# Kernel tuning notes

Hardware: AMD Instinct MI355X
Metric: run time of the kernel (lower is better)

Reference implementation:

```python
import jax, jax.numpy as jnp
import numpy as np

NUM_HEADS = 16


def setup_inputs() -> dict:
    key = jax.random.key(0)
    ks = jax.random.split(key, 6)
    B, N, M, C = 2, 2048, 2048, 1024
    return {
        "reference_data": jax.random.normal(ks[0], (B, N, C), dtype=jnp.float32),
        "target_data": jax.random.normal(ks[1], (B, M, C), dtype=jnp.float32),
        "Wq": jax.random.normal(ks[2], (C, C), dtype=jnp.float32) * (C ** -0.5),
        "Wkv": jax.random.normal(ks[3], (C, 2 * C), dtype=jnp.float32) * (C ** -0.5),
        "Wproj": jax.random.normal(ks[4], (C, C), dtype=jnp.float32) * (C ** -0.5),
        "bproj": jnp.zeros((C,), dtype=jnp.float32),
    }


def reference(reference_data, target_data, Wq, Wkv, Wproj, bproj):
    B, N, C = reference_data.shape
    M = target_data.shape[1]
    H = NUM_HEADS
    hd = C // H
    scale = hd ** -0.5
    # k, v from reference: [B, N, 2, H, hd] -> two [B, H, N, hd]
    kv = (reference_data @ Wkv).reshape(B, N, 2, H, hd)
    k = jnp.transpose(kv[:, :, 0], (0, 2, 1, 3))  # [B,H,N,hd]
    v = jnp.transpose(kv[:, :, 1], (0, 2, 1, 3))  # [B,H,N,hd]
    # q from target: [B, H, M, hd]
    q = jnp.transpose((target_data @ Wq).reshape(B, M, H, hd), (0, 2, 1, 3))
    attn = jnp.einsum("bhid,bhjd->bhij", q, k) * scale  # [B,H,M,N]
    attn = jax.nn.softmax(attn, axis=-1)
    x = jnp.einsum("bhij,bhjd->bhid", attn, v)  # [B,H,M,hd]
    x = jnp.transpose(x, (0, 2, 1, 3)).reshape(B, M, C)
    return x @ Wproj + bproj
```

## Files before the change

kernel.cpp:

```cpp
#include <hip/hip_runtime.h>
#include <hip/hip_bf16.h>
#include <stdint.h>

#define SEQ   2048
#define CH    1024
#define NH    16
#define HD    64
#define NUMEL (2 * NH * SEQ * HD)

typedef short bf8 __attribute__((ext_vector_type(8)));
typedef short bf4 __attribute__((ext_vector_type(4)));
typedef float f4  __attribute__((ext_vector_type(4)));
typedef unsigned short u16;

#define GAS(p) ((const __attribute__((address_space(1))) void*)(p))
#define LAS(p) ((__attribute__((address_space(3))) void*)(p))

__device__ __forceinline__ u16 f2bf(float f) {
  uint32_t u = __float_as_uint(f);
  u += 0x7fffu + ((u >> 16) & 1u);
  return (u16)(u >> 16);
}

__device__ __forceinline__ float bf2f(u16 v) {
  return __uint_as_float(((uint32_t)v) << 16);
}

__device__ __forceinline__ uint32_t pk2bf(float a, float b) {
  float2 f; f.x = a; f.y = b;
  __hip_bfloat162 h = __float22bfloat162_rn(f);
  union { __hip_bfloat162 h; uint32_t u; } cv; cv.h = h;
  return cv.u;
}

__device__ __forceinline__ f4 MFMA32(bf8 a, bf8 b, f4 c) {
  return __builtin_amdgcn_mfma_f32_16x16x32_bf16(a, b, c, 0, 0, 0);
}

__device__ __forceinline__ f4 MFMA16(bf4 a, bf4 b, f4 c) {
#if __has_builtin(__builtin_amdgcn_mfma_f32_16x16x16_bf16)
  return __builtin_amdgcn_mfma_f32_16x16x16_bf16(a, b, c, 0, 0, 0);
#elif __has_builtin(__builtin_amdgcn_mfma_f32_16x16x16bf16_1k)
  return __builtin_amdgcn_mfma_f32_16x16x16bf16_1k(a, b, c, 0, 0, 0);
#else
  f4 d = c;
  asm volatile("v_mfma_f32_16x16x16_bf16 %0, %1, %2, %0"
               : "+v"(d) : "v"(a), "v"(b));
  return d;
#endif
}

__global__ void prep(const float* __restrict__ ref, u16* __restrict__ refb,
                     const float* __restrict__ tgt, u16* __restrict__ tgtb,
                     const float* __restrict__ Wq, u16* __restrict__ Wqt,
                     const float* __restrict__ Wkv, u16* __restrict__ Wkvt,
                     const float* __restrict__ Wp, u16* __restrict__ Wpt) {
  __shared__ float tile[32][33];
  int blk = blockIdx.x;
  int t = threadIdx.x;
  if (blk < 8192) {
    const float* in; u16* out;
    if (blk < 4096) { in = ref; out = refb; } else { in = tgt; out = tgtb; blk -= 4096; }
    int i = (blk * 256 + t) * 4;
    float4 f = *reinterpret_cast<const float4*>(in + i);
    ushort4 o;
    o.x = f2bf(f.x); o.y = f2bf(f.y); o.z = f2bf(f.z); o.w = f2bf(f.w);
    *reinterpret_cast<ushort4*>(out + i) = o;
    return;
  }
  blk -= 8192;
  int x = blk & 127, by = blk >> 7;
  const float* in; u16* out; int N;
  if (x < 32)       { in = Wq;  out = Wqt;  N = CH;     }
  else if (x < 96)  { in = Wkv; out = Wkvt; N = 2 * CH; x -= 32; }
  else              { in = Wp;  out = Wpt;  N = CH;     x -= 96; }
  const int K = CH;
  int bn = x * 32, bk = by * 32;
  int tx = t & 31, ty = t >> 5;
  #pragma unroll
  for (int i = ty; i < 32; i += 8)
    tile[i][tx] = in[(size_t)(bk + i) * N + bn + tx];
  __syncthreads();
  #pragma unroll
  for (int i = ty; i < 32; i += 8)
    out[(size_t)(bn + i) * K + bk + tx] = f2bf(tile[tx][i]);
}

__global__ __launch_bounds__(256, 3)
void gemm_qkv(const u16* __restrict__ tgtb, const u16* __restrict__ refb,
              const u16* __restrict__ Wqt, const u16* __restrict__ Wkvt,
              u16* __restrict__ qb, u16* __restrict__ karr, u16* __restrict__ varr)
{
  __shared__ __align__(16) u16 As[2][4096];
  __shared__ __align__(16) u16 Bs[2][4096];
  const int tid = threadIdx.x;
  const int lane = tid & 63, wave = tid >> 6;
  const int l16 = lane & 15, q = lane >> 4;
  const int blk = blockIdx.x;
  const int n_idx = blk >> 5, m_idx = blk & 31;
  const bool isQ = n_idx >= 16;
  const u16* A  = isQ ? tgtb : refb;
  const u16* Bt = isQ ? Wqt : Wkvt;
  const int n0 = (isQ ? (n_idx - 16) : n_idx) * 128;
  const int m0 = m_idx * 128;
  const int wm = (wave >> 1) * 64, wn = (wave & 1) * 64;
  const int Kdim = CH;
  const int c = tid, c2 = tid + 256;
  const int ar = c >> 2, ac = (c & 3) << 3, ar2 = c2 >> 2, ac2 = (c2 & 3) << 3;

  f4 acc[4][4] = {};

  #define STAGE_G(buf, k0)                                                      \
    { __builtin_amdgcn_global_load_lds(                                         \
          GAS(&A[(size_t)(m0 + ar) * Kdim + (k0) + ac]),                        \
          LAS(&As[buf][c << 3]), 16, 0, 0);                                     \
      __builtin_amdgcn_global_load_lds(                                         \
          GAS(&A[(size_t)(m0 + ar2) * Kdim + (k0) + ac2]),                      \
          LAS(&As[buf][c2 << 3]), 16, 0, 0);                                    \
      __builtin_amdgcn_global_load_lds(                                         \
          GAS(&Bt[(size_t)(n0 + ar) * Kdim + (k0) + ac]),                       \
          LAS(&Bs[buf][c << 3]), 16, 0, 0);                                     \
      __builtin_amdgcn_global_load_lds(                                         \
          GAS(&Bt[(size_t)(n0 + ar2) * Kdim + (k0) + ac2]),                     \
          LAS(&Bs[buf][c2 << 3]), 16, 0, 0); }

  STAGE_G(0, 0);
  for (int kk = 0; kk < 32; ++kk) {
    __syncthreads();
    if (kk < 31) STAGE_G((kk + 1) & 1, (kk + 1) * 32);
    const u16* as = As[kk & 1];
    const u16* bs = Bs[kk & 1];
    bf8 a[4], b[4];
    #pragma unroll
    for (int i = 0; i < 4; ++i)
      a[i] = *reinterpret_cast<const bf8*>(&as[(wm + i * 16 + l16) * 32 + q * 8]);
    #pragma unroll
    for (int j = 0; j < 4; ++j)
      b[j] = *reinterpret_cast<const bf8*>(&bs[(wn + j * 16 + l16) * 32 + q * 8]);
    #pragma unroll
    for (int i = 0; i < 4; ++i)
      #pragma unroll
      for (int j = 0; j < 4; ++j)
        acc[i][j] = MFMA32(a[i], b[j], acc[i][j]);
  }
  #undef STAGE_G

  #pragma unroll
  for (int i = 0; i < 4; ++i) {
    const int mbase = m0 + wm + i * 16 + q * 4;
    const int b = mbase >> 11, ns0 = mbase & (SEQ - 1);
    #pragma unroll
    for (int j = 0; j < 4; ++j) {
      const int n = n0 + wn + j * 16 + l16;
      if (isQ) {
        int h = n >> 6, d = n & 63;
        #pragma unroll
        for (int r = 0; r < 4; ++r)
          qb[(size_t)((b * NH + h) * SEQ + ns0 + r) * HD + d] =
              f2bf(acc[i][j][r] * 0.1803368801f);
      } else if (n < CH) {
        int h = n >> 6, d = n & 63;
        size_t base = (size_t)(b * NH + h) * SEQ * HD;
        int off = (((ns0 >> 4) * 2 + (d >> 5)) * 4 + ((d >> 3) & 3)) * 128
                  + (d & 7);
        #pragma unroll
        for (int r = 0; r < 4; ++r)
          karr[base + off + ((ns0 + r) & 15) * 8] = f2bf(acc[i][j][r]);
      } else {
        int c2v = n - CH, h = c2v >> 6, d = c2v & 63;
        size_t base = (size_t)(b * NH + h) * SEQ * HD;
        int off = (((ns0 >> 4) * 2 + (d >> 5)) * 4 + ((ns0 >> 2) & 3)) * 128
                  + (d & 15) * 8 + ((d >> 4) & 1) * 4;
        ushort4 st;
        st.x = f2bf(acc[i][j][0]); st.y = f2bf(acc[i][j][1]);
        st.z = f2bf(acc[i][j][2]); st.w = f2bf(acc[i][j][3]);
        *reinterpret_cast<ushort4*>(&varr[base + off]) = st;
      }
    }
  }
}

__global__ __launch_bounds__(256, 2)
void gemm_proj(const u16* __restrict__ A, const u16* __restrict__ Bt,
               float* __restrict__ fo, const float* __restrict__ bias)
{
  __shared__ __align__(16) u16 As[2][2048];
  __shared__ __align__(16) u16 Bs[2][4096];
  const int tid = threadIdx.x;
  const int lane = tid & 63, wave = tid >> 6;
  const int l16 = lane & 15, q = lane >> 4;
  const int blk = blockIdx.x;
  const int m0 = (blk & 63) * 64, n0 = (blk >> 6) * 128;
  const int wm = (wave >> 1) * 32, wn = (wave & 1) * 64;
  const int Kdim = CH;
  const int c = tid, c2 = tid + 256;
  const int ar = c >> 2, ac = (c & 3) << 3, ar2 = c2 >> 2, ac2 = (c2 & 3) << 3;
  const int aar = c >> 2, aac = (c & 3) << 3;

  f4 acc[2][4] = {};

  #define STAGE_P(buf, k0)                                                      \
    { __builtin_amdgcn_global_load_lds(                                         \
          GAS(&A[(size_t)(m0 + aar) * Kdim + (k0) + aac]),                      \
          LAS(&As[buf][c << 3]), 16, 0, 0);                                     \
      __builtin_amdgcn_global_load_lds(                                         \
          GAS(&Bt[(size_t)(n0 + ar) * Kdim + (k0) + ac]),                       \
          LAS(&Bs[buf][c << 3]), 16, 0, 0);                                     \
      __builtin_amdgcn_global_load_lds(                                         \
          GAS(&Bt[(size_t)(n0 + ar2) * Kdim + (k0) + ac2]),                     \
          LAS(&Bs[buf][c2 << 3]), 16, 0, 0); }

  STAGE_P(0, 0);
  for (int kk = 0; kk < 32; ++kk) {
    __syncthreads();
    if (kk < 31) STAGE_P((kk + 1) & 1, (kk + 1) * 32);
    const u16* as = As[kk & 1];
    const u16* bs = Bs[kk & 1];
    bf8 a[2], b[4];
    #pragma unroll
    for (int i = 0; i < 2; ++i)
      a[i] = *reinterpret_cast<const bf8*>(&as[(wm + i * 16 + l16) * 32 + q * 8]);
    #pragma unroll
    for (int j = 0; j < 4; ++j)
      b[j] = *reinterpret_cast<const bf8*>(&bs[(wn + j * 16 + l16) * 32 + q * 8]);
    #pragma unroll
    for (int i = 0; i < 2; ++i)
      #pragma unroll
      for (int j = 0; j < 4; ++j)
        acc[i][j] = MFMA32(a[i], b[j], acc[i][j]);
  }
  #undef STAGE_P

  #pragma unroll
  for (int i = 0; i < 2; ++i) {
    const int mbase = m0 + wm + i * 16 + q * 4;
    #pragma unroll
    for (int j = 0; j < 4; ++j) {
      const int n = n0 + wn + j * 16 + l16;
      #pragma unroll
      for (int r = 0; r < 4; ++r)
        fo[(size_t)(mbase + r) * CH + n] = acc[i][j][r] + bias[n];
    }
  }
}

__global__ __launch_bounds__(512, 8)
void attn(const u16* __restrict__ Q, const u16* __restrict__ Karr,
          const u16* __restrict__ Varr, u16* __restrict__ num,
          float* __restrict__ den)
{
  __shared__ __align__(16) u16 Ks[8192];
  __shared__ __align__(16) u16 Vs[8192];
  const int tid = threadIdx.x;
  const int lane = tid & 63;
  const int l16 = lane & 15, q = lane >> 4;
  const int bh = blockIdx.y;
  const int m0 = blockIdx.x * 128;
  const int sp = blockIdx.z;
  const int wm = (tid >> 6) * 16;

  const u16* Qb = Q    + (size_t)bh * SEQ * HD;
  const u16* Kb = Karr + (size_t)bh * SEQ * HD;
  const u16* Vb = Varr + (size_t)bh * SEQ * HD;

  bf8 qf[2];
  #pragma unroll
  for (int ks = 0; ks < 2; ++ks)
    qf[ks] = *reinterpret_cast<const bf8*>(
        &Qb[(size_t)(m0 + wm + l16) * HD + ks * 32 + q * 8]);

  const short one_bf = 0x3F80;
  const bf4 ones = {one_bf, one_bf, one_bf, one_bf};

  f4 o[4] = {};
  f4 ds = {};

  const int t0 = sp * 8;
  for (int t = 0; t < 8; ++t) {
    const int tt = t0 + t;
    __syncthreads();
    {
      const u16* kg = Kb + (size_t)tt * 8192;
      const u16* vg = Vb + (size_t)tt * 8192;
      #pragma unroll
      for (int s = 0; s < 2; ++s) {
        int cc = tid + s * 512;
        __builtin_amdgcn_global_load_lds(GAS(kg + cc * 8), LAS(&Ks[cc * 8]), 16, 0, 0);
        __builtin_amdgcn_global_load_lds(GAS(vg + cc * 8), LAS(&Vs[cc * 8]), 16, 0, 0);
      }
    }
    __syncthreads();

    bf4 pa[8];
    #pragma unroll
    for (int j = 0; j < 8; ++j) {
      bf8 kf0 = *reinterpret_cast<const bf8*>(&Ks[((j * 2 + 0) * 4 + q) * 128 + l16 * 8]);
      bf8 kf1 = *reinterpret_cast<const bf8*>(&Ks[((j * 2 + 1) * 4 + q) * 128 + l16 * 8]);
      f4 z = {};
      z = MFMA32(kf0, qf[0], z);
      z = MFMA32(kf1, qf[1], z);
      union { bf4 v; uint32_t u[2]; } w;
      w.u[0] = pk2bf(exp2f(z[0]), exp2f(z[1]));
      w.u[1] = pk2bf(exp2f(z[2]), exp2f(z[3]));
      pa[j] = w.v;
    }

    #pragma unroll
    for (int j = 0; j < 8; ++j) {
      ds = MFMA16(pa[j], ones, ds);
      #pragma unroll
      for (int dh = 0; dh < 2; ++dh) {
        bf8 vv = *reinterpret_cast<const bf8*>(&Vs[((j * 2 + dh) * 4 + q) * 128 + l16 * 8]);
        bf4 v0 = __builtin_shufflevector(vv, vv, 0, 1, 2, 3);
        bf4 v1 = __builtin_shufflevector(vv, vv, 4, 5, 6, 7);
        o[dh * 2 + 0] = MFMA16(pa[j], v0, o[dh * 2 + 0]);
        o[dh * 2 + 1] = MFMA16(pa[j], v1, o[dh * 2 + 1]);
      }
    }
  }

  u16* nh = num + (size_t)sp * NUMEL;
  float* dh_ = den + (size_t)sp * (2 * NH * SEQ);
  #pragma unroll
  for (int r = 0; r < 4; ++r) {
    int m = m0 + wm + q * 4 + r;
    if (l16 == 0) dh_[bh * SEQ + m] = ds[r];
    #pragma unroll
    for (int dt = 0; dt < 4; ++dt)
      nh[((size_t)bh * SEQ + m) * HD + dt * 16 + l16] = f2bf(o[dt][r]);
  }
}

__global__ void combine(const u16* __restrict__ num, const float* __restrict__ den,
                        u16* __restrict__ xb) {
  int idx = (blockIdx.x * 256 + threadIdx.x) * 4;
  int bh = idx >> 17;
  int rem = idx & (SEQ * HD - 1);
  int m = rem >> 6, d = rem & 63;
  ushort4 a = *reinterpret_cast<const ushort4*>(num + idx);
  ushort4 b4 = *reinterpret_cast<const ushort4*>(num + NUMEL + idx);
  float dsum = den[bh * SEQ + m] + den[2 * NH * SEQ + bh * SEQ + m];
  float inv = 1.0f / dsum;
  int b = bh >> 4, h = bh & (NH - 1);
  ushort4 o;
  o.x = f2bf((bf2f(a.x) + bf2f(b4.x)) * inv);
  o.y = f2bf((bf2f(a.y) + bf2f(b4.y)) * inv);
  o.z = f2bf((bf2f(a.z) + bf2f(b4.z)) * inv);
  o.w = f2bf((bf2f(a.w) + bf2f(b4.w)) * inv);
  *reinterpret_cast<ushort4*>(&xb[(size_t)(b * SEQ + m) * CH + h * HD + d]) = o;
}

extern "C" void kernel_launch(void* const* d_in, const int* in_sizes, int n_in,
                              void* d_out, int out_size, void* d_ws, size_t ws_size,
                              hipStream_t stream) {
  const float* ref   = (const float*)d_in[0];
  const float* tgt   = (const float*)d_in[1];
  const float* Wq    = (const float*)d_in[2];
  const float* Wkv   = (const float*)d_in[3];
  const float* Wproj = (const float*)d_in[4];
  const float* bproj = (const float*)d_in[5];
  float* out = (float*)d_out;

  char* ws = (char*)d_ws;
  u16* refb = (u16*)(ws);
  u16* tgtb = (u16*)(ws + (8  << 20));
  u16* Wqt  = (u16*)(ws + (16 << 20));
  u16* Wkvt = (u16*)(ws + (18 << 20));
  u16* Wpt  = (u16*)(ws + (22 << 20));
  u16* qb   = (u16*)(ws + (24 << 20));
  u16* karr = (u16*)(ws + (32 << 20));
  u16* varr = (u16*)(ws + (40 << 20));
  u16* xb   = (u16*)(ws + (48 << 20));
  u16* nbuf  = refb;
  float* dbuf = (float*)Wqt;

  prep<<<12288, 256, 0, stream>>>(ref, refb, tgt, tgtb, Wq, Wqt, Wkv, Wkvt, Wproj, Wpt);

  gemm_qkv<<<768, 256, 0, stream>>>(tgtb, refb, Wqt, Wkvt, qb, karr, varr);

  attn<<<dim3(16, 32, 2), 512, 0, stream>>>(qb, karr, varr, nbuf, dbuf);

  combine<<<4096, 256, 0, stream>>>(nbuf, dbuf, xb);

  gemm_proj<<<512, 256, 0, stream>>>(xb, Wpt, out, bproj);
}
```

Before: 217.2 us.

## Rebalance QKV GEMM to 512 threads and double attention rows per wave

The QKV GEMM now runs 512 threads per block, so each wave computes a 32x64 sub-tile and each thread issues a single staging load per operand. The attention kernel now has each wave handle two 16-row query groups over 256 query rows per block. This halves the number of blocks and reuses each K/V tile loaded into LDS for twice as many queries. The cost is more registers per thread in attention (occupancy hint lowered from 8 to 4) and fewer blocks to spread across the GPU.

```diff
diff --git a/kernel.cpp b/kernel.cpp
--- a/kernel.cpp
+++ b/kernel.cpp
@@ -86,7 +86,7 @@
     out[(size_t)(bn + i) * K + bk + tx] = f2bf(tile[tx][i]);
 }
 
-__global__ __launch_bounds__(256, 3)
+__global__ __launch_bounds__(512, 6)
 void gemm_qkv(const u16* __restrict__ tgtb, const u16* __restrict__ refb,
               const u16* __restrict__ Wqt, const u16* __restrict__ Wkvt,
               u16* __restrict__ qb, u16* __restrict__ karr, u16* __restrict__ varr)
@@ -103,26 +103,19 @@
   const u16* Bt = isQ ? Wqt : Wkvt;
   const int n0 = (isQ ? (n_idx - 16) : n_idx) * 128;
   const int m0 = m_idx * 128;
-  const int wm = (wave >> 1) * 64, wn = (wave & 1) * 64;
+  const int wm = (wave >> 1) * 32, wn = (wave & 1) * 64;
   const int Kdim = CH;
-  const int c = tid, c2 = tid + 256;
-  const int ar = c >> 2, ac = (c & 3) << 3, ar2 = c2 >> 2, ac2 = (c2 & 3) << 3;
-
-  f4 acc[4][4] = {};
+  const int ar = tid >> 2, ac = (tid & 3) << 3;
+
+  f4 acc[2][4] = {};
 
   #define STAGE_G(buf, k0)                                                      \
     { __builtin_amdgcn_global_load_lds(                                         \
           GAS(&A[(size_t)(m0 + ar) * Kdim + (k0) + ac]),                        \
-          LAS(&As[buf][c << 3]), 16, 0, 0);                                     \
-      __builtin_amdgcn_global_load_lds(                                         \
-          GAS(&A[(size_t)(m0 + ar2) * Kdim + (k0) + ac2]),                      \
-          LAS(&As[buf][c2 << 3]), 16, 0, 0);                                    \
+          LAS(&As[buf][tid << 3]), 16, 0, 0);                                   \
       __builtin_amdgcn_global_load_lds(                                         \
           GAS(&Bt[(size_t)(n0 + ar) * Kdim + (k0) + ac]),                       \
-          LAS(&Bs[buf][c << 3]), 16, 0, 0);                                     \
-      __builtin_amdgcn_global_load_lds(                                         \
-          GAS(&Bt[(size_t)(n0 + ar2) * Kdim + (k0) + ac2]),                     \
-          LAS(&Bs[buf][c2 << 3]), 16, 0, 0); }
+          LAS(&Bs[buf][tid << 3]), 16, 0, 0); }
 
   STAGE_G(0, 0);
   for (int kk = 0; kk < 32; ++kk) {
@@ -130,15 +123,15 @@
     if (kk < 31) STAGE_G((kk + 1) & 1, (kk + 1) * 32);
     const u16* as = As[kk & 1];
     const u16* bs = Bs[kk & 1];
-    bf8 a[4], b[4];
-    #pragma unroll
-    for (int i = 0; i < 4; ++i)
+    bf8 a[2], b[4];
+    #pragma unroll
+    for (int i = 0; i < 2; ++i)
       a[i] = *reinterpret_cast<const bf8*>(&as[(wm + i * 16 + l16) * 32 + q * 8]);
     #pragma unroll
     for (int j = 0; j < 4; ++j)
       b[j] = *reinterpret_cast<const bf8*>(&bs[(wn + j * 16 + l16) * 32 + q * 8]);
     #pragma unroll
-    for (int i = 0; i < 4; ++i)
+    for (int i = 0; i < 2; ++i)
       #pragma unroll
       for (int j = 0; j < 4; ++j)
         acc[i][j] = MFMA32(a[i], b[j], acc[i][j]);
@@ -146,7 +139,7 @@
   #undef STAGE_G
 
   #pragma unroll
-  for (int i = 0; i < 4; ++i) {
+  for (int i = 0; i < 2; ++i) {
     const int mbase = m0 + wm + i * 16 + q * 4;
     const int b = mbase >> 11, ns0 = mbase & (SEQ - 1);
     #pragma unroll
@@ -244,7 +237,7 @@
   }
 }
 
-__global__ __launch_bounds__(512, 8)
+__global__ __launch_bounds__(512, 4)
 void attn(const u16* __restrict__ Q, const u16* __restrict__ Karr,
           const u16* __restrict__ Varr, u16* __restrict__ num,
           float* __restrict__ den)
@@ -255,25 +248,27 @@
   const int lane = tid & 63;
   const int l16 = lane & 15, q = lane >> 4;
   const int bh = blockIdx.y;
-  const int m0 = blockIdx.x * 128;
+  const int m0 = blockIdx.x * 256;
   const int sp = blockIdx.z;
-  const int wm = (tid >> 6) * 16;
+  const int wm = (tid >> 6) * 32;
 
   const u16* Qb = Q    + (size_t)bh * SEQ * HD;
   const u16* Kb = Karr + (size_t)bh * SEQ * HD;
   const u16* Vb = Varr + (size_t)bh * SEQ * HD;
 
-  bf8 qf[2];
-  #pragma unroll
-  for (int ks = 0; ks < 2; ++ks)
-    qf[ks] = *reinterpret_cast<const bf8*>(
-        &Qb[(size_t)(m0 + wm + l16) * HD + ks * 32 + q * 8]);
+  bf8 qf[2][2];
+  #pragma unroll
+  for (int i = 0; i < 2; ++i)
+    #pragma unroll
+    for (int ks = 0; ks < 2; ++ks)
+      qf[i][ks] = *reinterpret_cast<const bf8*>(
+          &Qb[(size_t)(m0 + wm + i * 16 + l16) * HD + ks * 32 + q * 8]);
 
   const short one_bf = 0x3F80;
   const bf4 ones = {one_bf, one_bf, one_bf, one_bf};
 
-  f4 o[4] = {};
-  f4 ds = {};
+  f4 o[2][4] = {};
+  f4 ds[2] = {};
 
   const int t0 = sp * 8;
   for (int t = 0; t < 8; ++t) {
@@ -291,30 +286,38 @@
     }
     __syncthreads();
 
-    bf4 pa[8];
+    bf4 pa[2][8];
     #pragma unroll
     for (int j = 0; j < 8; ++j) {
       bf8 kf0 = *reinterpret_cast<const bf8*>(&Ks[((j * 2 + 0) * 4 + q) * 128 + l16 * 8]);
       bf8 kf1 = *reinterpret_cast<const bf8*>(&Ks[((j * 2 + 1) * 4 + q) * 128 + l16 * 8]);
-      f4 z = {};
-      z = MFMA32(kf0, qf[0], z);
-      z = MFMA32(kf1, qf[1], z);
-      union { bf4 v; uint32_t u[2]; } w;
-      w.u[0] = pk2bf(exp2f(z[0]), exp2f(z[1]));
-      w.u[1] = pk2bf(exp2f(z[2]), exp2f(z[3]));
-      pa[j] = w.v;
+      #pragma unroll
+      for (int i = 0; i < 2; ++i) {
+        f4 z = {};
+        z = MFMA32(kf0, qf[i][0], z);
+        z = MFMA32(kf1, qf[i][1], z);
+        union { bf4 v; uint32_t u[2]; } w;
+        w.u[0] = pk2bf(exp2f(z[0]), exp2f(z[1]));
+        w.u[1] = pk2bf(exp2f(z[2]), exp2f(z[3]));
+        pa[i][j] = w.v;
+      }
     }
 
     #pragma unroll
     for (int j = 0; j < 8; ++j) {
-      ds = MFMA16(pa[j], ones, ds);
+      #pragma unroll
+      for (int i = 0; i < 2; ++i)
+        ds[i] = MFMA16(pa[i][j], ones, ds[i]);
       #pragma unroll
       for (int dh = 0; dh < 2; ++dh) {
         bf8 vv = *reinterpret_cast<const bf8*>(&Vs[((j * 2 + dh) * 4 + q) * 128 + l16 * 8]);
         bf4 v0 = __builtin_shufflevector(vv, vv, 0, 1, 2, 3);
         bf4 v1 = __builtin_shufflevector(vv, vv, 4, 5, 6, 7);
-        o[dh * 2 + 0] = MFMA16(pa[j], v0, o[dh * 2 + 0]);
-        o[dh * 2 + 1] = MFMA16(pa[j], v1, o[dh * 2 + 1]);
+        #pragma unroll
+        for (int i = 0; i < 2; ++i) {
+          o[i][dh * 2 + 0] = MFMA16(pa[i][j], v0, o[i][dh * 2 + 0]);
+          o[i][dh * 2 + 1] = MFMA16(pa[i][j], v1, o[i][dh * 2 + 1]);
+        }
       }
     }
   }
@@ -322,13 +325,15 @@
   u16* nh = num + (size_t)sp * NUMEL;
   float* dh_ = den + (size_t)sp * (2 * NH * SEQ);
   #pragma unroll
-  for (int r = 0; r < 4; ++r) {
-    int m = m0 + wm + q * 4 + r;
-    if (l16 == 0) dh_[bh * SEQ + m] = ds[r];
-    #pragma unroll
-    for (int dt = 0; dt < 4; ++dt)
-      nh[((size_t)bh * SEQ + m) * HD + dt * 16 + l16] = f2bf(o[dt][r]);
-  }
+  for (int i = 0; i < 2; ++i)
+    #pragma unroll
+    for (int r = 0; r < 4; ++r) {
+      int m = m0 + wm + i * 16 + q * 4 + r;
+      if (l16 == 0) dh_[bh * SEQ + m] = ds[i][r];
+      #pragma unroll
+      for (int dt = 0; dt < 4; ++dt)
+        nh[((size_t)bh * SEQ + m) * HD + dt * 16 + l16] = f2bf(o[i][dt][r]);
+    }
 }
 
 __global__ void combine(const u16* __restrict__ num, const float* __restrict__ den,
@@ -376,9 +381,9 @@
 
   prep<<<12288, 256, 0, stream>>>(ref, refb, tgt, tgtb, Wq, Wqt, Wkv, Wkvt, Wproj, Wpt);
 
-  gemm_qkv<<<768, 256, 0, stream>>>(tgtb, refb, Wqt, Wkvt, qb, karr, varr);
-
-  attn<<<dim3(16, 32, 2), 512, 0, stream>>>(qb, karr, varr, nbuf, dbuf);
+  gemm_qkv<<<768, 512, 0, stream>>>(tgtb, refb, Wqt, Wkvt, qb, karr, varr);
+
+  attn<<<dim3(8, 32, 2), 512, 0, stream>>>(qb, karr, varr, nbuf, dbuf);
 
   combine<<<4096, 256, 0, stream>>>(nbuf, dbuf, xb);
 
```

After: 218.2 us. About the same (+0.4%).
